# Kernel optimization log

Measured on AMD Instinct MI355X. Metric: run time of the kernel, lower is better.

## Reference

```python
import jax, jax.numpy as jnp
import numpy as np

TEMPERATURE = 1.0
NEG = -1e9
EPS = 1e-8


def setup_inputs() -> dict:
    key = jax.random.key(0)
    k1, k2, k3 = jax.random.split(key, 3)
    B, H = 524288, 32
    scores = jax.random.normal(k1, (B, H), dtype=jnp.float32)
    rankings = jax.random.randint(k2, (B, H), 0, 33, dtype=jnp.int32)
    mask = jax.random.randint(k3, (B, H), 0, 2, dtype=jnp.int32).astype(bool)
    return {"scores": scores, "rankings": rankings, "mask": mask}


def reference(scores, rankings, mask):
    B, H = scores.shape
    # effective validity: horse present AND has a ranking > 0 (top_k=None)
    m = mask & (rankings > 0)
    # masked, temperature-scaled scores; -1e9 entries underflow to exactly 0 in softmax
    s = jnp.where(m, scores / TEMPERATURE, NEG)
    p = jax.nn.softmax(s, axis=1)  # [B, H], ~0 at invalid slots

    n_valid = jnp.sum(m, axis=1)  # [B]
    # ideal order: valid horses sorted by ranking ascending (invalid pushed to end)
    rank_key = jnp.where(m, rankings, jnp.iinfo(jnp.int32).max)
    rank_order = jnp.argsort(rank_key, axis=1)          # stable sort
    # prediction order: valid horses in original index order (matches torch.where)
    pos_order = jnp.argsort(~m, axis=1)                 # stable: valid first

    q = jnp.take_along_axis(p, rank_order, axis=1)      # ideal_probs, aligned by list position
    pr = jnp.take_along_axis(p, pos_order, axis=1)      # pred_probs,  aligned by list position

    # positions >= n_valid are padding
    valid_pos = jnp.arange(H)[None, :] < n_valid[:, None]
    q_safe = jnp.where(valid_pos, q, 1.0)
    pr_safe = jnp.where(valid_pos, pr, 1.0)
    # KL(ideal || pred) with the original's log(pred + 1e-8)
    kl_terms = q_safe * (jnp.log(q_safe) - jnp.log(pr_safe + EPS))
    kl = jnp.sum(jnp.where(valid_pos, kl_terms, 0.0), axis=1)  # [B]

    # rows with <= 1 valid ranked horse are skipped entirely
    row_ok = n_valid > 1
    n_rows = jnp.maximum(jnp.sum(row_ok), 1)
    return jnp.sum(jnp.where(row_ok, kl, 0.0)) / n_rows  # reduction='mean'
```

## Files before the change

kernel.cpp:

```cpp
#include <hip/hip_runtime.h>
#include <stdint.h>


#define SWZ(x, pat) __int_as_float(__builtin_amdgcn_ds_swizzle(__float_as_int(x), pat))

__device__ __forceinline__ float rowsum32(float x) {
    x += SWZ(x, 0x041F);
    x += SWZ(x, 0x081F);
    x += SWZ(x, 0x101F);
    x += SWZ(x, 0x201F);
    x += SWZ(x, 0x401F);
    return x;
}

__global__ __launch_bounds__(256) void listwise_kernel(
    const float* __restrict__ scores,
    const int* __restrict__ rankings,
    const unsigned char* __restrict__ mask_u8,
    float* __restrict__ ws_kl,
    int* __restrict__ ws_cnt,
    int npairs)
{
    const int lane = threadIdx.x & 63;
    const int gl   = lane & 31;
    const int sh   = lane & 32;
    const bool hi_half = (sh != 0);
    const uint32_t lmask = (1u << gl) - 1u;
    const int wid = threadIdx.x >> 6;
    const int wavesPerBlock = blockDim.x >> 6;
    const int gw = blockIdx.x * wavesPerBlock + wid;
    const int totWaves = gridDim.x * wavesPerBlock;

    unsigned char probe = mask_u8[lane];
    const bool mask_is_i32 =
        (__ballot(((lane & 3) != 0) && (probe != 0)) == 0ull);
    const int* mask_i32 = (const int*)mask_u8;

    float th_kl = 0.0f;
    int   th_cnt = 0;

    for (int pair = gw; pair < npairs; pair += totWaves) {
        const int base = pair * 64 + lane;
        const float s = scores[base];
        const int   r = rankings[base];
        const int   mk = mask_is_i32 ? mask_i32[base] : (int)mask_u8[base];
        const bool valid = (mk != 0) && (r > 0);

        const unsigned long long balv = __ballot(valid);
        const uint32_t vm = hi_half ? (uint32_t)(balv >> 32) : (uint32_t)balv;
        const int nv = __popc(vm);

        const float e = valid ? __expf(s) : 0.0f;
        const float se = rowsum32(e);

        const uint32_t v = ((uint32_t)(r - 1)) & 31u;
        uint32_t E = vm;
        int c_lt = 0;
        #pragma unroll
        for (int i = 4; i >= 0; --i) {
            const uint32_t t = (v >> i) & 1u;
            const unsigned long long bb = __ballot(t != 0u);
            const uint32_t bi = hi_half ? (uint32_t)(bb >> 32) : (uint32_t)bb;
            c_lt += t ? __popc(E & ~bi) : 0;
            E &= t ? bi : ~bi;
        }
        const int j_rank = c_lt + __popc(E & lmask);
        const int j_pos  = __popc(vm & lmask);

        const int dst = valid ? j_pos : (nv + (gl - j_pos));
        const int scat = __builtin_amdgcn_ds_permute((sh + dst) << 2,
                                                     __float_as_int(s));
        const int gidx = valid ? j_rank : 0;
        const float g = __int_as_float(
            __builtin_amdgcn_ds_bpermute((sh + gidx) << 2, scat));

        const float t1 = e * (s - g);
        const float num = rowsum32(t1);

        if (gl == 0 && nv > 1) {
            th_kl += __fdividef(num, se);
            th_cnt += 1;
        }
    }

    #pragma unroll
    for (int m = 32; m >= 1; m >>= 1) {
        th_kl  += __shfl_xor(th_kl, m);
        th_cnt += __shfl_xor(th_cnt, m);
    }
    __shared__ float s_kl[8];
    __shared__ int   s_cnt[8];
    if (lane == 0) { s_kl[wid] = th_kl; s_cnt[wid] = th_cnt; }
    __syncthreads();
    if (threadIdx.x == 0) {
        float k = 0.0f; int c = 0;
        for (int i = 0; i < wavesPerBlock; ++i) { k += s_kl[i]; c += s_cnt[i]; }
        atomicAdd(ws_kl, k);
        atomicAdd(ws_cnt, c);
    }
}

__global__ void finalize_kernel(const float* __restrict__ ws_kl,
                                const int* __restrict__ ws_cnt,
                                float* __restrict__ out)
{
    if (threadIdx.x == 0) {
        int c = *ws_cnt;
        if (c < 1) c = 1;
        out[0] = *ws_kl / (float)c;
    }
}

extern "C" void kernel_launch(void* const* d_in, const int* in_sizes, int n_in,
                              void* d_out, int out_size, void* d_ws, size_t ws_size,
                              hipStream_t stream) {
    const float* scores = (const float*)d_in[0];
    const int* rankings = (const int*)d_in[1];
    const unsigned char* mask = (const unsigned char*)d_in[2];
    float* out = (float*)d_out;

    const int total = in_sizes[0];
    const int npairs = total / 64;

    float* wsf = (float*)d_ws;
    int*   wsi = (int*)d_ws;

    hipMemsetAsync(d_ws, 0, 8, stream);

    const int threads = 256;
    const int blocks = 2048;
    listwise_kernel<<<blocks, threads, 0, stream>>>(
        scores, rankings, mask, wsf, wsi + 1, npairs);

    finalize_kernel<<<1, 64, 0, stream>>>(wsf, wsi + 1, out);
}
```

Measured before the change: 240.6 us.

## Use DPP row reductions and process two row-pairs per loop iteration

Replaces the ds_swizzle butterfly reductions with DPP row_shr/row_bcast adds that leave each 32-lane half's sum in lane 31, and moves the per-row accumulation to that lane. The main loop is also unrolled by two, issuing the loads for two 64-element pairs before computing either, so more memory requests are in flight per wave. The cost is higher register pressure. The DPP row_bcast15 pattern has to merge the 16-lane rows correctly for the sums to be right.

```diff
diff --git a/kernel.cpp b/kernel.cpp
--- a/kernel.cpp
+++ b/kernel.cpp
@@ -2,14 +2,18 @@
 #include <stdint.h>
 
 
-#define SWZ(x, pat) __int_as_float(__builtin_amdgcn_ds_swizzle(__float_as_int(x), pat))
+template <int CTRL>
+__device__ __forceinline__ float dpp_add(float x) {
+    int t = __builtin_amdgcn_update_dpp(0, __float_as_int(x), CTRL, 0xf, 0xf, true);
+    return x + __int_as_float(t);
+}
 
-__device__ __forceinline__ float rowsum32(float x) {
-    x += SWZ(x, 0x041F);
-    x += SWZ(x, 0x081F);
-    x += SWZ(x, 0x101F);
-    x += SWZ(x, 0x201F);
-    x += SWZ(x, 0x401F);
+__device__ __forceinline__ float rowsum32_lane31(float x) {
+    x = dpp_add<0x111>(x);
+    x = dpp_add<0x112>(x);
+    x = dpp_add<0x114>(x);
+    x = dpp_add<0x118>(x);
+    x = dpp_add<0x142>(x);
     return x;
 }
 
@@ -39,47 +43,59 @@
     float th_kl = 0.0f;
     int   th_cnt = 0;
 
-    for (int pair = gw; pair < npairs; pair += totWaves) {
-        const int base = pair * 64 + lane;
-        const float s = scores[base];
-        const int   r = rankings[base];
-        const int   mk = mask_is_i32 ? mask_i32[base] : (int)mask_u8[base];
-        const bool valid = (mk != 0) && (r > 0);
+    for (int pair0 = gw * 2; pair0 < npairs; pair0 += totWaves * 2) {
+        float sv[2]; int rv[2]; int mkv[2];
+        #pragma unroll
+        for (int u = 0; u < 2; ++u) {
+            const int pair = pair0 + u;
+            if (pair < npairs) {
+                const int base = pair * 64 + lane;
+                sv[u]  = scores[base];
+                rv[u]  = rankings[base];
+                mkv[u] = mask_is_i32 ? mask_i32[base] : (int)mask_u8[base];
+            } else { sv[u] = 0.0f; rv[u] = 0; mkv[u] = 0; }
+        }
 
-        const unsigned long long balv = __ballot(valid);
-        const uint32_t vm = hi_half ? (uint32_t)(balv >> 32) : (uint32_t)balv;
-        const int nv = __popc(vm);
+        #pragma unroll
+        for (int u = 0; u < 2; ++u) {
+            const float s = sv[u];
+            const int   r = rv[u];
+            const bool valid = (mkv[u] != 0) && (r > 0);
 
-        const float e = valid ? __expf(s) : 0.0f;
-        const float se = rowsum32(e);
+            const unsigned long long balv = __ballot(valid);
+            const uint32_t vm = hi_half ? (uint32_t)(balv >> 32) : (uint32_t)balv;
+            const int nv = __popc(vm);
 
-        const uint32_t v = ((uint32_t)(r - 1)) & 31u;
-        uint32_t E = vm;
-        int c_lt = 0;
-        #pragma unroll
-        for (int i = 4; i >= 0; --i) {
-            const uint32_t t = (v >> i) & 1u;
-            const unsigned long long bb = __ballot(t != 0u);
-            const uint32_t bi = hi_half ? (uint32_t)(bb >> 32) : (uint32_t)bb;
-            c_lt += t ? __popc(E & ~bi) : 0;
-            E &= t ? bi : ~bi;
-        }
-        const int j_rank = c_lt + __popc(E & lmask);
-        const int j_pos  = __popc(vm & lmask);
+            const float e = valid ? __expf(s) : 0.0f;
+            const float se = rowsum32_lane31(e);
 
-        const int dst = valid ? j_pos : (nv + (gl - j_pos));
-        const int scat = __builtin_amdgcn_ds_permute((sh + dst) << 2,
-                                                     __float_as_int(s));
-        const int gidx = valid ? j_rank : 0;
-        const float g = __int_as_float(
-            __builtin_amdgcn_ds_bpermute((sh + gidx) << 2, scat));
+            const uint32_t v = ((uint32_t)(r - 1)) & 31u;
+            uint32_t E = vm;
+            int c_lt = 0;
+            #pragma unroll
+            for (int i = 4; i >= 0; --i) {
+                const uint32_t t = (v >> i) & 1u;
+                const unsigned long long bb = __ballot(t != 0u);
+                const uint32_t bi = hi_half ? (uint32_t)(bb >> 32) : (uint32_t)bb;
+                c_lt += t ? __popc(E & ~bi) : 0;
+                E &= t ? bi : ~bi;
+            }
+            const int j_rank = c_lt + __popc(E & lmask);
+            const int j_pos  = __popc(vm & lmask);
 
-        const float t1 = e * (s - g);
-        const float num = rowsum32(t1);
+            const int dst = valid ? j_pos : (nv + (gl - j_pos));
+            const int scat = __builtin_amdgcn_ds_permute((sh + dst) << 2,
+                                                         __float_as_int(s));
+            const int gidx = valid ? j_rank : 0;
+            const float g = __int_as_float(
+                __builtin_amdgcn_ds_bpermute((sh + gidx) << 2, scat));
 
-        if (gl == 0 && nv > 1) {
-            th_kl += __fdividef(num, se);
-            th_cnt += 1;
+            const float num = rowsum32_lane31(e * (s - g));
+
+            if (gl == 31 && nv > 1) {
+                th_kl += __fdividef(num, se);
+                th_cnt += 1;
+            }
         }
     }
 
```

New measurement: 228.1 us. -5.2%, faster.
